# Kernel tuning notes

Hardware: AMD Instinct MI355X
Metric: run time of the kernel (lower is better)

Reference implementation:

```python
import jax, jax.numpy as jnp
import numpy as np

B, L, D, V, K = 4, 2048, 1024, 32, 4096  # batch, seq, embedding_dim, vq_dim, num_embeddings


def setup_inputs() -> dict:
    key = jax.random.key(0)
    k0, k1, k2, k3 = jax.random.split(key, 4)
    h = jax.random.normal(k0, (B, L, D), jnp.float32)
    attn_mask = jnp.ones((B, L), jnp.float32)
    # proj: Linear(D -> V); proj_inv: Linear(V -> D)
    Wp = jax.random.normal(k1, (V, D), jnp.float32) / np.float32(np.sqrt(D))
    bp = jnp.zeros((V,), jnp.float32)
    Wpi = jax.random.normal(k2, (D, V), jnp.float32) / np.float32(np.sqrt(V))
    bpi = jnp.zeros((D,), jnp.float32)
    # embedding init uniform(-1/K, 1/K)
    emb = jax.random.uniform(k3, (K, V), jnp.float32, -1.0 / K, 1.0 / K)
    return {"h": h, "attn_mask": attn_mask, "Wp": Wp, "bp": bp,
            "Wpi": Wpi, "bpi": bpi, "emb": emb}


def reference(h, attn_mask, Wp, bp, Wpi, bpi, emb, temperature=1.0):
    # project + L2 normalize
    hp = jnp.einsum('bld,vd->blv', h, Wp) + bp            # [B,L,V]
    hp = hp / jnp.linalg.norm(hp, axis=-1, keepdims=True)
    # normalize codebook (in torch this is an in-place .data update)
    emb_n = emb / jnp.linalg.norm(emb, axis=-1, keepdims=True)  # [K,V]
    # squared euclidean distances hp vs codebook
    d = (jnp.sum(hp * hp, axis=-1, keepdims=True)
         + jnp.sum(emb_n * emb_n, axis=-1)
         - 2.0 * jnp.einsum('blv,kv->blk', hp, emb_n))    # [B,L,K]
    A = jax.nn.softmax(-d / temperature, axis=-1)         # [B,L,K]
    code = jnp.argmax(A, axis=-1)                         # [B,L]
    h_vq = jnp.einsum('blk,kv->blv', A, emb_n)            # train mode: A @ embedding
    # masked scatter into zeros is equivalent to masking out unselected positions
    m = (attn_mask == 1)
    quantized = jnp.where(m[..., None], h_vq, jnp.float32(0.0))
    vq_code = jnp.where(m, code, 0).astype(jnp.int32)
    quantized = jnp.einsum('blv,dv->bld', quantized, Wpi) + bpi
    vq_loss = jnp.float32(0.0)
    return quantized, vq_code, vq_loss
```

## Files before the change

### kernel.cpp

```cpp
#include <hip/hip_runtime.h>
#include <hip/hip_bf16.h>
#include <math.h>

#define NTOK 8192
#define DIM  1024
#define VDIM 32
#define KCODES 4096

#define SC 2.8853900817779268f

typedef __attribute__((ext_vector_type(8))) short short8;
typedef __attribute__((ext_vector_type(4))) float f32x4;
typedef __attribute__((ext_vector_type(2))) float f32x2;

#define MFMA16(A,B,C) __builtin_amdgcn_mfma_f32_16x16x32_bf16(A, B, C, 0, 0, 0)

__device__ __forceinline__ unsigned short f2bf(float x) {
    unsigned u = __builtin_bit_cast(unsigned, x);
    u += 0x7FFF + ((u >> 16) & 1);
    return (unsigned short)(u >> 16);
}
__device__ __forceinline__ float bf2f(unsigned short b) {
    unsigned u = ((unsigned)b) << 16;
    return __builtin_bit_cast(float, u);
}
__device__ __forceinline__ float fexp2(float x) {
#if __has_builtin(__builtin_amdgcn_exp2f)
    return __builtin_amdgcn_exp2f(x);
#else
    return __expf(0.6931471805599453f * x);
#endif
}

struct U4 { unsigned x, y, z, w; };

__device__ __forceinline__ void split8(const float* p, short8* H, short8* L) {
    unsigned hh[4], ll[4];
    #pragma unroll
    for (int i = 0; i < 4; ++i) {
        unsigned short a = f2bf(p[2 * i]);
        unsigned short b = f2bf(p[2 * i + 1]);
        hh[i] = (unsigned)a | ((unsigned)b << 16);
        unsigned short la = f2bf(p[2 * i] - bf2f(a));
        unsigned short lb = f2bf(p[2 * i + 1] - bf2f(b));
        ll[i] = (unsigned)la | ((unsigned)lb << 16);
    }
    U4 uh = {hh[0], hh[1], hh[2], hh[3]};
    U4 ul = {ll[0], ll[1], ll[2], ll[3]};
    *H = __builtin_bit_cast(short8, uh);
    *L = __builtin_bit_cast(short8, ul);
}

__device__ __forceinline__ short8 pack8(const float* p) {
    unsigned u[8];
    #pragma unroll
    for (int j = 0; j < 8; ++j) u[j] = __builtin_bit_cast(unsigned, p[j]) + 0x8000u;
    U4 uh;
    uh.x = __builtin_amdgcn_perm(u[1], u[0], 0x07060302);
    uh.y = __builtin_amdgcn_perm(u[3], u[2], 0x07060302);
    uh.z = __builtin_amdgcn_perm(u[5], u[4], 0x07060302);
    uh.w = __builtin_amdgcn_perm(u[7], u[6], 0x07060302);
    return __builtin_bit_cast(short8, uh);
}

__device__ __forceinline__ int lsw(int row, int j) {
    int s = ((row >> 1) ^ (row >> 3)) & 3;
    return row * 40 + ((j ^ s) * 8);
}

#define OFS_E_HI   0
#define OFS_E_LO   131072
#define OFS_ET_HI  262144
#define OFS_WP_HI  393216
#define OFS_WP_LO  425984
#define OFS_WPI_HI 458752
#define OFS_WPI_LO 491520
#define OFS_HP_HI  524288
#define OFS_HP_LO  786432
#define F32_BASE   1048576
#define NSPLIT 8
#define FOFS_HVP 0
#define FOFS_LP  2097152
#define FOFS_AMP 2162688
#define FOFS_AIP 2228224

__global__ __launch_bounds__(256) void k_prep(const float* __restrict__ emb,
                                              const float* __restrict__ Wp,
                                              const float* __restrict__ Wpi,
                                              unsigned short* __restrict__ W,
                                              float* __restrict__ loss_out) {
    __shared__ __align__(16) unsigned short Th[32][72];
    int bid = blockIdx.x, tid = threadIdx.x;
    if (bid < 64) {
        int cb = bid * 64;
        int c = tid >> 2, s = tid & 3;
        const float* src = emb + (size_t)(cb + c) * VDIM + s * 8;
        float4 a = *(const float4*)src;
        float4 b = *(const float4*)(src + 4);
        float ps = a.x*a.x + a.y*a.y + a.z*a.z + a.w*a.w
                 + b.x*b.x + b.y*b.y + b.z*b.z + b.w*b.w;
        ps += __shfl_xor(ps, 1);
        ps += __shfl_xor(ps, 2);
        float inv = 1.0f / sqrtf(ps);
        float vals[8] = {a.x*inv, a.y*inv, a.z*inv, a.w*inv,
                         b.x*inv, b.y*inv, b.z*inv, b.w*inv};
        short8 H, L;
        split8(vals, &H, &L);
        *(short8*)(W + OFS_E_HI + (size_t)(cb + c) * VDIM + s * 8) = H;
        *(short8*)(W + OFS_E_LO + (size_t)(cb + c) * VDIM + s * 8) = L;
        #pragma unroll
        for (int j = 0; j < 8; ++j) Th[s * 8 + j][c] = f2bf(vals[j]);
        __syncthreads();
        int row = tid >> 3, seg = tid & 7;
        *(short8*)(W + OFS_ET_HI + (size_t)row * KCODES + cb + seg * 8) =
            *(const short8*)&Th[row][seg * 8];
        if (bid == 0 && tid == 0) loss_out[0] = 0.0f;
    } else if (bid < 80) {
        int i0 = (bid - 64) * 2048 + tid * 8;
        float4 a = *(const float4*)(Wp + i0);
        float4 b = *(const float4*)(Wp + i0 + 4);
        float vals[8] = {a.x, a.y, a.z, a.w, b.x, b.y, b.z, b.w};
        short8 H, L;
        split8(vals, &H, &L);
        *(short8*)(W + OFS_WP_HI + i0) = H;
        *(short8*)(W + OFS_WP_LO + i0) = L;
    } else {
        int i0 = (bid - 80) * 2048 + tid * 8;
        float4 a = *(const float4*)(Wpi + i0);
        float4 b = *(const float4*)(Wpi + i0 + 4);
        float vals[8] = {a.x, a.y, a.z, a.w, b.x, b.y, b.z, b.w};
        short8 H, L;
        split8(vals, &H, &L);
        *(short8*)(W + OFS_WPI_HI + i0) = H;
        *(short8*)(W + OFS_WPI_LO + i0) = L;
    }
}

__global__ __launch_bounds__(256) void k_proj(const float* __restrict__ h,
                                              const unsigned short* __restrict__ W,
                                              const float* __restrict__ bp,
                                              unsigned short* __restrict__ hp_hi,
                                              unsigned short* __restrict__ hp_lo) {
    __shared__ __align__(16) float red[4][16][36];
    const unsigned short* Wp_hi = W + OFS_WP_HI;
    const unsigned short* Wp_lo = W + OFS_WP_LO;
    int tid = threadIdx.x;
    int w = tid >> 6, l = tid & 63, q = l >> 4, m = l & 15;
    int tok0 = blockIdx.x * 16;
    const f32x4 zero4 = {0.f, 0.f, 0.f, 0.f};
    f32x4 acc0 = zero4, acc1 = zero4;
    const float* hb = h + (size_t)(tok0 + m) * DIM + w * 256 + q * 8;
    const unsigned short* w0h = Wp_hi + (size_t)m * DIM + w * 256 + q * 8;
    const unsigned short* w0l = Wp_lo + (size_t)m * DIM + w * 256 + q * 8;
    const unsigned short* w1h = w0h + (size_t)16 * DIM;
    const unsigned short* w1l = w0l + (size_t)16 * DIM;
    #pragma unroll
    for (int c = 0; c < 8; ++c) {
        float4 a = *(const float4*)(hb + c * 32);
        float4 b = *(const float4*)(hb + c * 32 + 4);
        float va[8] = {a.x, a.y, a.z, a.w, b.x, b.y, b.z, b.w};
        short8 Bh, Bl;
        split8(va, &Bh, &Bl);
        short8 A0h = *(const short8*)(w0h + c * 32);
        short8 A0l = *(const short8*)(w0l + c * 32);
        short8 A1h = *(const short8*)(w1h + c * 32);
        short8 A1l = *(const short8*)(w1l + c * 32);
        acc0 = MFMA16(A0l, Bl, acc0); acc0 = MFMA16(A0l, Bh, acc0);
        acc0 = MFMA16(A0h, Bl, acc0); acc0 = MFMA16(A0h, Bh, acc0);
        acc1 = MFMA16(A1l, Bl, acc1); acc1 = MFMA16(A1l, Bh, acc1);
        acc1 = MFMA16(A1h, Bl, acc1); acc1 = MFMA16(A1h, Bh, acc1);
    }
    *(f32x4*)&red[w][m][4 * q]      = acc0;
    *(f32x4*)&red[w][m][16 + 4 * q] = acc1;
    __syncthreads();
    #pragma unroll
    for (int half = 0; half < 2; ++half) {
        int t = (tid >> 5) + half * 8, v = tid & 31;
        float s = bp[v];
        #pragma unroll
        for (int j = 0; j < 4; ++j) s += red[j][t][v];
        float sq = s * s;
        #pragma unroll
        for (int off = 1; off < 32; off <<= 1) sq += __shfl_xor(sq, off);
        float nv = s * (SC / sqrtf(sq));
        unsigned short hb2 = f2bf(nv);
        size_t idx = (size_t)(tok0 + t) * VDIM + v;
        hp_hi[idx] = hb2;
        hp_lo[idx] = f2bf(nv - bf2f(hb2));
    }
}

__global__ __launch_bounds__(256, 2) void k_vq(const unsigned short* __restrict__ W,
                                               float* __restrict__ hvp,
                                               float* __restrict__ lp,
                                               float* __restrict__ amp,
                                               int* __restrict__ aip) {
    __shared__ __align__(16) unsigned short Eh[2][64 * 40];
    __shared__ __align__(16) unsigned short El[2][64 * 40];

    const unsigned short* E_hi  = W + OFS_E_HI;
    const unsigned short* E_lo  = W + OFS_E_LO;
    const unsigned short* Et_hi = W + OFS_ET_HI;
    const unsigned short* hp_hi = W + OFS_HP_HI;
    const unsigned short* hp_lo = W + OFS_HP_LO;

    int tid = threadIdx.x;
    int w = tid >> 6, l = tid & 63, q = l >> 4, m = l & 15;
    int tg = blockIdx.x >> 3, sp = blockIdx.x & 7;
    int tok0 = tg * 128 + w * 32;
    int cb0 = sp * 512;
    int sig = ((m & 12) << 1) | (m & 3);
    const f32x4 zero4 = {0.f, 0.f, 0.f, 0.f};

    int cs = tid >> 2, js = tid & 3;
    int lds_off = lsw(cs, js);
    size_t gs = (size_t)cs * VDIM + js * 8;

    size_t h0 = (size_t)(tok0 + m) * VDIM + q * 8;
    short8 hph0 = *(const short8*)(hp_hi + h0);
    short8 hpl0 = *(const short8*)(hp_lo + h0);
    short8 hph1 = *(const short8*)(hp_hi + h0 + 16 * VDIM);
    short8 hpl1 = *(const short8*)(hp_lo + h0 + 16 * VDIM);

    {
        size_t tb = (size_t)cb0 * VDIM;
        short8 a = *(const short8*)(E_hi + tb + gs);
        short8 b = *(const short8*)(E_lo + tb + gs);
        *(short8*)&Eh[0][lds_off] = a;
        *(short8*)&El[0][lds_off] = b;
    }
    __syncthreads();

    f32x4 hv00 = zero4, hv01 = zero4, hv10 = zero4, hv11 = zero4;
    f32x2 ls0v = {0.f, 0.f}, ls1v = {0.f, 0.f};
    float am0 = -1e30f, am1 = -1e30f;
    int ai0 = 0, ai1 = 0;

    #pragma unroll 1
    for (int t = 0; t < 8; ++t) {
        int buf = t & 1;
        short8 sa, sb;
        if (t < 7) {
            size_t tb = (size_t)(cb0 + (t + 1) * 64) * VDIM;
            sa = *(const short8*)(E_hi + tb + gs);
            sb = *(const short8*)(E_lo + tb + gs);
        }
        int cbase = cb0 + t * 64;
        size_t tb0 = (size_t)sig * KCODES + cbase + q * 8;
        short8 T00 = *(const short8*)(Et_hi + tb0);
        short8 T01 = *(const short8*)(Et_hi + tb0 + (size_t)4 * KCODES);
        short8 T10 = *(const short8*)(Et_hi + tb0 + 32);
        short8 T11 = *(const short8*)(Et_hi + tb0 + 32 + (size_t)4 * KCODES);
        short8 E00h = *(const short8*)&Eh[buf][lsw(sig,          q)];
        short8 E00l = *(const short8*)&El[buf][lsw(sig,          q)];
        short8 E01h = *(const short8*)&Eh[buf][lsw(sig + 4,      q)];
        short8 E01l = *(const short8*)&El[buf][lsw(sig + 4,      q)];
        short8 E10h = *(const short8*)&Eh[buf][lsw(32 + sig,     q)];
        short8 E10l = *(const short8*)&El[buf][lsw(32 + sig,     q)];
        short8 E11h = *(const short8*)&Eh[buf][lsw(32 + sig + 4, q)];
        short8 E11l = *(const short8*)&El[buf][lsw(32 + sig + 4, q)];

        f32x4 sA0, sA1, sB0, sB1, sC0, sC1, sD0, sD1;
        sA0 = MFMA16(E00h, hpl0, zero4);
        sA1 = MFMA16(E01h, hpl0, zero4);
        sB0 = MFMA16(E00h, hpl1, zero4);
        sB1 = MFMA16(E01h, hpl1, zero4);
        sC0 = MFMA16(E10h, hpl0, zero4);
        sC1 = MFMA16(E11h, hpl0, zero4);
        sD0 = MFMA16(E10h, hpl1, zero4);
        sD1 = MFMA16(E11h, hpl1, zero4);
        sA0 = MFMA16(E00l, hph0, sA0);
        sA1 = MFMA16(E01l, hph0, sA1);
        sB0 = MFMA16(E00l, hph1, sB0);
        sB1 = MFMA16(E01l, hph1, sB1);
        sC0 = MFMA16(E10l, hph0, sC0);
        sC1 = MFMA16(E11l, hph0, sC1);
        sD0 = MFMA16(E10l, hph1, sD0);
        sD1 = MFMA16(E11l, hph1, sD1);
        sA0 = MFMA16(E00h, hph0, sA0);
        sA1 = MFMA16(E01h, hph0, sA1);
        sB0 = MFMA16(E00h, hph1, sB0);
        sB1 = MFMA16(E01h, hph1, sB1);
        sC0 = MFMA16(E10h, hph0, sC0);
        sC1 = MFMA16(E11h, hph0, sC1);
        sD0 = MFMA16(E10h, hph1, sD0);
        sD1 = MFMA16(E11h, hph1, sD1);

        {
            int lbase = cbase + 8 * q;
            float p[8];
            #pragma unroll
            for (int r = 0; r < 4; ++r) { p[r] = fexp2(sA0[r]); p[4 + r] = fexp2(sA1[r]); }
            short8 Ph = pack8(p);
            hv00 = MFMA16(T00, Ph, hv00);
            hv01 = MFMA16(T01, Ph, hv01);
            #pragma unroll
            for (int r = 0; r < 4; ++r) {
                float sv = sA0[r];
                if (sv > am0) { am0 = sv; ai0 = lbase + r; }
                sv = sA1[r];
                if (sv > am0) { am0 = sv; ai0 = lbase + 4 + r; }
            }
            f32x2 pa = {p[0], p[1]}, pb = {p[2], p[3]};
            f32x2 pc = {p[4], p[5]}, pd = {p[6], p[7]};
            ls0v += (pa + pb) + (pc + pd);
        }
        {
            int lbase = cbase + 8 * q;
            float p[8];
            #pragma unroll
            for (int r = 0; r < 4; ++r) { p[r] = fexp2(sB0[r]); p[4 + r] = fexp2(sB1[r]); }
            short8 Ph = pack8(p);
            hv10 = MFMA16(T00, Ph, hv10);
            hv11 = MFMA16(T01, Ph, hv11);
            #pragma unroll
            for (int r = 0; r < 4; ++r) {
                float sv = sB0[r];
                if (sv > am1) { am1 = sv; ai1 = lbase + r; }
                sv = sB1[r];
                if (sv > am1) { am1 = sv; ai1 = lbase + 4 + r; }
            }
            f32x2 pa = {p[0], p[1]}, pb = {p[2], p[3]};
            f32x2 pc = {p[4], p[5]}, pd = {p[6], p[7]};
            ls1v += (pa + pb) + (pc + pd);
        }
        {
            int lbase = cbase + 32 + 8 * q;
            float p[8];
            #pragma unroll
            for (int r = 0; r < 4; ++r) { p[r] = fexp2(sC0[r]); p[4 + r] = fexp2(sC1[r]); }
            short8 Ph = pack8(p);
            hv00 = MFMA16(T10, Ph, hv00);
            hv01 = MFMA16(T11, Ph, hv01);
            #pragma unroll
            for (int r = 0; r < 4; ++r) {
                float sv = sC0[r];
                if (sv > am0) { am0 = sv; ai0 = lbase + r; }
                sv = sC1[r];
                if (sv > am0) { am0 = sv; ai0 = lbase + 4 + r; }
            }
            f32x2 pa = {p[0], p[1]}, pb = {p[2], p[3]};
            f32x2 pc = {p[4], p[5]}, pd = {p[6], p[7]};
            ls0v += (pa + pb) + (pc + pd);
        }
        {
            int lbase = cbase + 32 + 8 * q;
            float p[8];
            #pragma unroll
            for (int r = 0; r < 4; ++r) { p[r] = fexp2(sD0[r]); p[4 + r] = fexp2(sD1[r]); }
            short8 Ph = pack8(p);
            hv10 = MFMA16(T10, Ph, hv10);
            hv11 = MFMA16(T11, Ph, hv11);
            #pragma unroll
            for (int r = 0; r < 4; ++r) {
                float sv = sD0[r];
                if (sv > am1) { am1 = sv; ai1 = lbase + r; }
                sv = sD1[r];
                if (sv > am1) { am1 = sv; ai1 = lbase + 4 + r; }
            }
            f32x2 pa = {p[0], p[1]}, pb = {p[2], p[3]};
            f32x2 pc = {p[4], p[5]}, pd = {p[6], p[7]};
            ls1v += (pa + pb) + (pc + pd);
        }

        if (t < 7) {
            int nb = buf ^ 1;
            *(short8*)&Eh[nb][lds_off] = sa;
            *(short8*)&El[nb][lds_off] = sb;
            __syncthreads();
        }
    }

    float ls0 = ls0v.x + ls0v.y;
    float ls1 = ls1v.x + ls1v.y;
    #pragma unroll
    for (int off = 16; off <= 32; off <<= 1) {
        ls0 += __shfl_xor(ls0, off);
        float a2 = __shfl_xor(am0, off);
        int   i2 = __shfl_xor(ai0, off);
        if (a2 > am0 || (a2 == am0 && i2 < ai0)) { am0 = a2; ai0 = i2; }
        ls1 += __shfl_xor(ls1, off);
        a2 = __shfl_xor(am1, off);
        i2 = __shfl_xor(ai1, off);
        if (a2 > am1 || (a2 == am1 && i2 < ai1)) { am1 = a2; ai1 = i2; }
    }
    size_t gtok = (size_t)sp * NTOK + tok0;
    if (q == 0) {
        lp[gtok + m] = ls0;      amp[gtok + m] = am0;      aip[gtok + m] = ai0;
        lp[gtok + 16 + m] = ls1; amp[gtok + 16 + m] = am1; aip[gtok + 16 + m] = ai1;
    }
    float* dst0 = hvp + (gtok + m) * VDIM;
    *(f32x4*)(dst0 + 8 * q)     = hv00;
    *(f32x4*)(dst0 + 8 * q + 4) = hv01;
    float* dst1 = hvp + (gtok + 16 + m) * VDIM;
    *(f32x4*)(dst1 + 8 * q)     = hv10;
    *(f32x4*)(dst1 + 8 * q + 4) = hv11;
}

__global__ __launch_bounds__(256) void k_out(const unsigned short* __restrict__ W,
                                             const float* __restrict__ mask,
                                             const float* __restrict__ bpi,
                                             const float* __restrict__ hvp,
                                             const float* __restrict__ lp,
                                             const float* __restrict__ amp,
                                             const int* __restrict__ aip,
                                             float* __restrict__ out,
                                             float* __restrict__ code_out) {
    __shared__ float invl[16];
    __shared__ float lred[16][9];
    __shared__ float amred[16][9];
    __shared__ int   aired[16][9];
    __shared__ __align__(16) unsigned short hvh[16][40];
    __shared__ __align__(16) unsigned short hvl[16][40];
    const unsigned short* Wpi_hi = W + OFS_WPI_HI;
    const unsigned short* Wpi_lo = W + OFS_WPI_LO;
    int tid = threadIdx.x;
    int tok0 = blockIdx.x * 16;
    const f32x4 zero4 = {0.f, 0.f, 0.f, 0.f};

    if (tid < 128) {
        int t = tid >> 3, s = tid & 7;
        size_t gi = (size_t)s * NTOK + tok0 + t;
        lred[t][s]  = lp[gi];
        amred[t][s] = amp[gi];
        aired[t][s] = aip[gi];
    }
    __syncthreads();
    if (tid < 16) {
        float L = 0.f, A = -1e30f;
        int I = 0x7fffffff;
        #pragma unroll
        for (int s = 0; s < NSPLIT; ++s) {
            L += lred[tid][s];
            float a2 = amred[tid][s];
            int   i2 = aired[tid][s];
            if (a2 > A || (a2 == A && i2 < I)) { A = a2; I = i2; }
        }
        bool on = (mask[tok0 + tid] == 1.0f);
        code_out[tok0 + tid] = on ? (float)I : 0.0f;
        invl[tid] = on ? (1.0f / L) : 0.0f;
    }
    __syncthreads();
    if (tid < 128) {
        int t = tid >> 3, g = tid & 7;
        f32x4 x = zero4;
        #pragma unroll
        for (int sp = 0; sp < NSPLIT; ++sp)
            x += *(const f32x4*)&hvp[((size_t)sp * NTOK + tok0 + t) * VDIM + g * 4];
        float iv = invl[t];
        #pragma unroll
        for (int j = 0; j < 4; ++j) {
            float xv = x[j] * iv;
            unsigned short hb = f2bf(xv);
            hvh[t][g * 4 + j] = hb;
            hvl[t][g * 4 + j] = f2bf(xv - bf2f(hb));
        }
    }
    __syncthreads();
    int w = tid >> 6, l = tid & 63, q = l >> 4, m = l & 15;
    short8 gh = *(const short8*)&hvh[m][q * 8];
    short8 gl = *(const short8*)&hvl[m][q * 8];
    #pragma unroll
    for (int dt = 0; dt < 16; ++dt) {
        int dbase = w * 256 + dt * 16;
        short8 Ah = *(const short8*)(Wpi_hi + (size_t)(dbase + m) * VDIM + q * 8);
        short8 Al = *(const short8*)(Wpi_lo + (size_t)(dbase + m) * VDIM + q * 8);
        f32x4 o = MFMA16(Al, gh, zero4);
        o = MFMA16(Ah, gl, o);
        o = MFMA16(Ah, gh, o);
        float4 bias = *(const float4*)(bpi + dbase + 4 * q);
        float4 r0 = make_float4(o[0] + bias.x, o[1] + bias.y,
                                o[2] + bias.z, o[3] + bias.w);
        *(float4*)(out + (size_t)(tok0 + m) * DIM + dbase + 4 * q) = r0;
    }
}

extern "C" void kernel_launch(void* const* d_in, const int* in_sizes, int n_in,
                              void* d_out, int out_size, void* d_ws, size_t ws_size,
                              hipStream_t stream) {
    const float* h    = (const float*)d_in[0];
    const float* mask = (const float*)d_in[1];
    const float* Wp   = (const float*)d_in[2];
    const float* bp   = (const float*)d_in[3];
    const float* Wpi  = (const float*)d_in[4];
    const float* bpi  = (const float*)d_in[5];
    const float* emb  = (const float*)d_in[6];
    float* out = (float*)d_out;

    unsigned short* W = (unsigned short*)d_ws;
    unsigned short* hp_hi = W + OFS_HP_HI;
    unsigned short* hp_lo = W + OFS_HP_LO;
    float* fbase = (float*)(W + F32_BASE);
    float* hvp = fbase + FOFS_HVP;
    float* lpp = fbase + FOFS_LP;
    float* ampp = fbase + FOFS_AMP;
    int*   aipp = (int*)(fbase + FOFS_AIP);

    float* code_out = out + (size_t)NTOK * DIM;
    float* loss_out = code_out + NTOK;

    hipLaunchKernelGGL(k_prep, dim3(96),  dim3(256), 0, stream, emb, Wp, Wpi, W, loss_out);
    hipLaunchKernelGGL(k_proj, dim3(512), dim3(256), 0, stream, h, W, bp, hp_hi, hp_lo);
    hipLaunchKernelGGL(k_vq,   dim3(512), dim3(256), 0, stream, W, hvp, lpp, ampp, aipp);
    hipLaunchKernelGGL(k_out,  dim3(512), dim3(256), 0, stream, W, mask, bpi, hvp, lpp, ampp, aipp, out, code_out);
}
```

Before: 134.1 us.

## Shrink prep kernel, fold codebook prep into proj, halve vq block size

```diff
diff --git a/kernel.cpp b/kernel.cpp
--- a/kernel.cpp
+++ b/kernel.cpp
@@ -84,67 +84,71 @@
 #define FOFS_AMP 2162688
 #define FOFS_AIP 2228224
 
-__global__ __launch_bounds__(256) void k_prep(const float* __restrict__ emb,
-                                              const float* __restrict__ Wp,
+__global__ __launch_bounds__(256) void k_prep(const float* __restrict__ Wp,
+                                              unsigned short* __restrict__ W,
+                                              float* __restrict__ loss_out) {
+    int bid = blockIdx.x, tid = threadIdx.x;
+    int i0 = bid * 2048 + tid * 8;
+    float4 a = *(const float4*)(Wp + i0);
+    float4 b = *(const float4*)(Wp + i0 + 4);
+    float vals[8] = {a.x, a.y, a.z, a.w, b.x, b.y, b.z, b.w};
+    short8 H, L;
+    split8(vals, &H, &L);
+    *(short8*)(W + OFS_WP_HI + i0) = H;
+    *(short8*)(W + OFS_WP_LO + i0) = L;
+    if (bid == 0 && tid == 0) loss_out[0] = 0.0f;
+}
+
+__global__ __launch_bounds__(256) void k_proj(const float* __restrict__ h,
+                                              const unsigned short* __restrict__ Wr,
+                                              const float* __restrict__ bp,
+                                              const float* __restrict__ emb,
                                               const float* __restrict__ Wpi,
                                               unsigned short* __restrict__ W,
-                                              float* __restrict__ loss_out) {
-    __shared__ __align__(16) unsigned short Th[32][72];
-    int bid = blockIdx.x, tid = threadIdx.x;
-    if (bid < 64) {
-        int cb = bid * 64;
-        int c = tid >> 2, s = tid & 3;
-        const float* src = emb + (size_t)(cb + c) * VDIM + s * 8;
-        float4 a = *(const float4*)src;
-        float4 b = *(const float4*)(src + 4);
-        float ps = a.x*a.x + a.y*a.y + a.z*a.z + a.w*a.w
-                 + b.x*b.x + b.y*b.y + b.z*b.z + b.w*b.w;
-        ps += __shfl_xor(ps, 1);
-        ps += __shfl_xor(ps, 2);
-        float inv = 1.0f / sqrtf(ps);
-        float vals[8] = {a.x*inv, a.y*inv, a.z*inv, a.w*inv,
-                         b.x*inv, b.y*inv, b.z*inv, b.w*inv};
-        short8 H, L;
-        split8(vals, &H, &L);
-        *(short8*)(W + OFS_E_HI + (size_t)(cb + c) * VDIM + s * 8) = H;
-        *(short8*)(W + OFS_E_LO + (size_t)(cb + c) * VDIM + s * 8) = L;
-        #pragma unroll
-        for (int j = 0; j < 8; ++j) Th[s * 8 + j][c] = f2bf(vals[j]);
-        __syncthreads();
-        int row = tid >> 3, seg = tid & 7;
-        *(short8*)(W + OFS_ET_HI + (size_t)row * KCODES + cb + seg * 8) =
-            *(const short8*)&Th[row][seg * 8];
-        if (bid == 0 && tid == 0) loss_out[0] = 0.0f;
-    } else if (bid < 80) {
-        int i0 = (bid - 64) * 2048 + tid * 8;
-        float4 a = *(const float4*)(Wp + i0);
-        float4 b = *(const float4*)(Wp + i0 + 4);
-        float vals[8] = {a.x, a.y, a.z, a.w, b.x, b.y, b.z, b.w};
-        short8 H, L;
-        split8(vals, &H, &L);
-        *(short8*)(W + OFS_WP_HI + i0) = H;
-        *(short8*)(W + OFS_WP_LO + i0) = L;
-    } else {
-        int i0 = (bid - 80) * 2048 + tid * 8;
-        float4 a = *(const float4*)(Wpi + i0);
-        float4 b = *(const float4*)(Wpi + i0 + 4);
-        float vals[8] = {a.x, a.y, a.z, a.w, b.x, b.y, b.z, b.w};
-        short8 H, L;
-        split8(vals, &H, &L);
-        *(short8*)(W + OFS_WPI_HI + i0) = H;
-        *(short8*)(W + OFS_WPI_LO + i0) = L;
-    }
-}
-
-__global__ __launch_bounds__(256) void k_proj(const float* __restrict__ h,
-                                              const unsigned short* __restrict__ W,
-                                              const float* __restrict__ bp,
                                               unsigned short* __restrict__ hp_hi,
                                               unsigned short* __restrict__ hp_lo) {
     __shared__ __align__(16) float red[4][16][36];
-    const unsigned short* Wp_hi = W + OFS_WP_HI;
-    const unsigned short* Wp_lo = W + OFS_WP_LO;
+    __shared__ __align__(16) unsigned short Th[32][72];
     int tid = threadIdx.x;
+    if (blockIdx.x >= 512) {
+        int bid2 = blockIdx.x - 512;
+        if (bid2 < 64) {
+            int cb = bid2 * 64;
+            int c = tid >> 2, s = tid & 3;
+            const float* src = emb + (size_t)(cb + c) * VDIM + s * 8;
+            float4 a = *(const float4*)src;
+            float4 b = *(const float4*)(src + 4);
+            float ps = a.x*a.x + a.y*a.y + a.z*a.z + a.w*a.w
+                     + b.x*b.x + b.y*b.y + b.z*b.z + b.w*b.w;
+            ps += __shfl_xor(ps, 1);
+            ps += __shfl_xor(ps, 2);
+            float inv = 1.0f / sqrtf(ps);
+            float vals[8] = {a.x*inv, a.y*inv, a.z*inv, a.w*inv,
+                             b.x*inv, b.y*inv, b.z*inv, b.w*inv};
+            short8 H, L;
+            split8(vals, &H, &L);
+            *(short8*)(W + OFS_E_HI + (size_t)(cb + c) * VDIM + s * 8) = H;
+            *(short8*)(W + OFS_E_LO + (size_t)(cb + c) * VDIM + s * 8) = L;
+            #pragma unroll
+            for (int j = 0; j < 8; ++j) Th[s * 8 + j][c] = f2bf(vals[j]);
+            __syncthreads();
+            int row = tid >> 3, seg = tid & 7;
+            *(short8*)(W + OFS_ET_HI + (size_t)row * KCODES + cb + seg * 8) =
+                *(const short8*)&Th[row][seg * 8];
+        } else {
+            int i0 = (bid2 - 64) * 2048 + tid * 8;
+            float4 a = *(const float4*)(Wpi + i0);
+            float4 b = *(const float4*)(Wpi + i0 + 4);
+            float vals[8] = {a.x, a.y, a.z, a.w, b.x, b.y, b.z, b.w};
+            short8 H, L;
+            split8(vals, &H, &L);
+            *(short8*)(W + OFS_WPI_HI + i0) = H;
+            *(short8*)(W + OFS_WPI_LO + i0) = L;
+        }
+        return;
+    }
+    const unsigned short* Wp_hi = Wr + OFS_WP_HI;
+    const unsigned short* Wp_lo = Wr + OFS_WP_LO;
     int w = tid >> 6, l = tid & 63, q = l >> 4, m = l & 15;
     int tok0 = blockIdx.x * 16;
     const f32x4 zero4 = {0.f, 0.f, 0.f, 0.f};
@@ -190,7 +194,7 @@
     }
 }
 
-__global__ __launch_bounds__(256, 2) void k_vq(const unsigned short* __restrict__ W,
+__global__ __launch_bounds__(128, 2) void k_vq(const unsigned short* __restrict__ W,
                                                float* __restrict__ hvp,
                                                float* __restrict__ lp,
                                                float* __restrict__ amp,
@@ -207,14 +211,15 @@
     int tid = threadIdx.x;
     int w = tid >> 6, l = tid & 63, q = l >> 4, m = l & 15;
     int tg = blockIdx.x >> 3, sp = blockIdx.x & 7;
-    int tok0 = tg * 128 + w * 32;
+    int tok0 = tg * 64 + w * 32;
     int cb0 = sp * 512;
     int sig = ((m & 12) << 1) | (m & 3);
     const f32x4 zero4 = {0.f, 0.f, 0.f, 0.f};
 
-    int cs = tid >> 2, js = tid & 3;
-    int lds_off = lsw(cs, js);
-    size_t gs = (size_t)cs * VDIM + js * 8;
+    int cs = tid >> 1, jb = (tid & 1) * 2;
+    int lds_o0 = lsw(cs, jb), lds_o1 = lsw(cs, jb + 1);
+    size_t gs0 = (size_t)cs * VDIM + jb * 8;
+    size_t gs1 = gs0 + 8;
 
     size_t h0 = (size_t)(tok0 + m) * VDIM + q * 8;
     short8 hph0 = *(const short8*)(hp_hi + h0);
@@ -224,10 +229,14 @@
 
     {
         size_t tb = (size_t)cb0 * VDIM;
-        short8 a = *(const short8*)(E_hi + tb + gs);
-        short8 b = *(const short8*)(E_lo + tb + gs);
-        *(short8*)&Eh[0][lds_off] = a;
-        *(short8*)&El[0][lds_off] = b;
+        short8 a0 = *(const short8*)(E_hi + tb + gs0);
+        short8 a1 = *(const short8*)(E_hi + tb + gs1);
+        short8 b0 = *(const short8*)(E_lo + tb + gs0);
+        short8 b1 = *(const short8*)(E_lo + tb + gs1);
+        *(short8*)&Eh[0][lds_o0] = a0;
+        *(short8*)&Eh[0][lds_o1] = a1;
+        *(short8*)&El[0][lds_o0] = b0;
+        *(short8*)&El[0][lds_o1] = b1;
     }
     __syncthreads();
 
@@ -239,11 +248,13 @@
     #pragma unroll 1
     for (int t = 0; t < 8; ++t) {
         int buf = t & 1;
-        short8 sa, sb;
+        short8 sa0, sa1, sb0, sb1;
         if (t < 7) {
             size_t tb = (size_t)(cb0 + (t + 1) * 64) * VDIM;
-            sa = *(const short8*)(E_hi + tb + gs);
-            sb = *(const short8*)(E_lo + tb + gs);
+            sa0 = *(const short8*)(E_hi + tb + gs0);
+            sa1 = *(const short8*)(E_hi + tb + gs1);
+            sb0 = *(const short8*)(E_lo + tb + gs0);
+            sb1 = *(const short8*)(E_lo + tb + gs1);
         }
         int cbase = cb0 + t * 64;
         size_t tb0 = (size_t)sig * KCODES + cbase + q * 8;
@@ -365,8 +376,10 @@
 
         if (t < 7) {
             int nb = buf ^ 1;
-            *(short8*)&Eh[nb][lds_off] = sa;
-            *(short8*)&El[nb][lds_off] = sb;
+            *(short8*)&Eh[nb][lds_o0] = sa0;
+            *(short8*)&Eh[nb][lds_o1] = sa1;
+            *(short8*)&El[nb][lds_o0] = sb0;
+            *(short8*)&El[nb][lds_o1] = sb1;
             __syncthreads();
         }
     }
@@ -499,8 +512,8 @@
     float* code_out = out + (size_t)NTOK * DIM;
     float* loss_out = code_out + NTOK;
 
-    hipLaunchKernelGGL(k_prep, dim3(96),  dim3(256), 0, stream, emb, Wp, Wpi, W, loss_out);
-    hipLaunchKernelGGL(k_proj, dim3(512), dim3(256), 0, stream, h, W, bp, hp_hi, hp_lo);
-    hipLaunchKernelGGL(k_vq,   dim3(512), dim3(256), 0, stream, W, hvp, lpp, ampp, aipp);
-    hipLaunchKernelGGL(k_out,  dim3(512), dim3(256), 0, stream, W, mask, bpi, hvp, lpp, ampp, aipp, out, code_out);
-}
+    hipLaunchKernelGGL(k_prep, dim3(16),   dim3(256), 0, stream, Wp, W, loss_out);
+    hipLaunchKernelGGL(k_proj, dim3(592),  dim3(256), 0, stream, h, W, bp, emb, Wpi, W, hp_hi, hp_lo);
+    hipLaunchKernelGGL(k_vq,   dim3(1024), dim3(128), 0, stream, W, hvp, lpp, ampp, aipp);
+    hipLaunchKernelGGL(k_out,  dim3(512),  dim3(256), 0, stream, W, mask, bpi, hvp, lpp, ampp, aipp, out, code_out);
+}
```

Measured after the change: 134.7 us. Within noise of the previous version (+0.5%).

## Fold prep kernel into projection and double tokens per output block

Applied to the files above, without the earlier changes.

```diff
diff --git a/kernel.cpp b/kernel.cpp
--- a/kernel.cpp
+++ b/kernel.cpp
@@ -71,8 +71,6 @@
 #define OFS_E_HI   0
 #define OFS_E_LO   131072
 #define OFS_ET_HI  262144
-#define OFS_WP_HI  393216
-#define OFS_WP_LO  425984
 #define OFS_WPI_HI 458752
 #define OFS_WPI_LO 491520
 #define OFS_HP_HI  524288
@@ -84,76 +82,63 @@
 #define FOFS_AMP 2162688
 #define FOFS_AIP 2228224
 
-__global__ __launch_bounds__(256) void k_prep(const float* __restrict__ emb,
+__global__ __launch_bounds__(256) void k_proj(const float* __restrict__ h,
                                               const float* __restrict__ Wp,
+                                              const float* __restrict__ bp,
+                                              const float* __restrict__ emb,
                                               const float* __restrict__ Wpi,
                                               unsigned short* __restrict__ W,
+                                              unsigned short* __restrict__ hp_hi,
+                                              unsigned short* __restrict__ hp_lo,
                                               float* __restrict__ loss_out) {
+    __shared__ __align__(16) float red[4][16][36];
     __shared__ __align__(16) unsigned short Th[32][72];
-    int bid = blockIdx.x, tid = threadIdx.x;
-    if (bid < 64) {
-        int cb = bid * 64;
-        int c = tid >> 2, s = tid & 3;
-        const float* src = emb + (size_t)(cb + c) * VDIM + s * 8;
-        float4 a = *(const float4*)src;
-        float4 b = *(const float4*)(src + 4);
-        float ps = a.x*a.x + a.y*a.y + a.z*a.z + a.w*a.w
-                 + b.x*b.x + b.y*b.y + b.z*b.z + b.w*b.w;
-        ps += __shfl_xor(ps, 1);
-        ps += __shfl_xor(ps, 2);
-        float inv = 1.0f / sqrtf(ps);
-        float vals[8] = {a.x*inv, a.y*inv, a.z*inv, a.w*inv,
-                         b.x*inv, b.y*inv, b.z*inv, b.w*inv};
-        short8 H, L;
-        split8(vals, &H, &L);
-        *(short8*)(W + OFS_E_HI + (size_t)(cb + c) * VDIM + s * 8) = H;
-        *(short8*)(W + OFS_E_LO + (size_t)(cb + c) * VDIM + s * 8) = L;
-        #pragma unroll
-        for (int j = 0; j < 8; ++j) Th[s * 8 + j][c] = f2bf(vals[j]);
-        __syncthreads();
-        int row = tid >> 3, seg = tid & 7;
-        *(short8*)(W + OFS_ET_HI + (size_t)row * KCODES + cb + seg * 8) =
-            *(const short8*)&Th[row][seg * 8];
-        if (bid == 0 && tid == 0) loss_out[0] = 0.0f;
-    } else if (bid < 80) {
-        int i0 = (bid - 64) * 2048 + tid * 8;
-        float4 a = *(const float4*)(Wp + i0);
-        float4 b = *(const float4*)(Wp + i0 + 4);
-        float vals[8] = {a.x, a.y, a.z, a.w, b.x, b.y, b.z, b.w};
-        short8 H, L;
-        split8(vals, &H, &L);
-        *(short8*)(W + OFS_WP_HI + i0) = H;
-        *(short8*)(W + OFS_WP_LO + i0) = L;
-    } else {
-        int i0 = (bid - 80) * 2048 + tid * 8;
-        float4 a = *(const float4*)(Wpi + i0);
-        float4 b = *(const float4*)(Wpi + i0 + 4);
-        float vals[8] = {a.x, a.y, a.z, a.w, b.x, b.y, b.z, b.w};
-        short8 H, L;
-        split8(vals, &H, &L);
-        *(short8*)(W + OFS_WPI_HI + i0) = H;
-        *(short8*)(W + OFS_WPI_LO + i0) = L;
-    }
-}
-
-__global__ __launch_bounds__(256) void k_proj(const float* __restrict__ h,
-                                              const unsigned short* __restrict__ W,
-                                              const float* __restrict__ bp,
-                                              unsigned short* __restrict__ hp_hi,
-                                              unsigned short* __restrict__ hp_lo) {
-    __shared__ __align__(16) float red[4][16][36];
-    const unsigned short* Wp_hi = W + OFS_WP_HI;
-    const unsigned short* Wp_lo = W + OFS_WP_LO;
     int tid = threadIdx.x;
+    if (blockIdx.x >= 512) {
+        int bid2 = blockIdx.x - 512;
+        if (bid2 < 64) {
+            int cb = bid2 * 64;
+            int c = tid >> 2, s = tid & 3;
+            const float* src = emb + (size_t)(cb + c) * VDIM + s * 8;
+            float4 a = *(const float4*)src;
+            float4 b = *(const float4*)(src + 4);
+            float ps = a.x*a.x + a.y*a.y + a.z*a.z + a.w*a.w
+                     + b.x*b.x + b.y*b.y + b.z*b.z + b.w*b.w;
+            ps += __shfl_xor(ps, 1);
+            ps += __shfl_xor(ps, 2);
+            float inv = 1.0f / sqrtf(ps);
+            float vals[8] = {a.x*inv, a.y*inv, a.z*inv, a.w*inv,
+                             b.x*inv, b.y*inv, b.z*inv, b.w*inv};
+            short8 H, L;
+            split8(vals, &H, &L);
+            *(short8*)(W + OFS_E_HI + (size_t)(cb + c) * VDIM + s * 8) = H;
+            *(short8*)(W + OFS_E_LO + (size_t)(cb + c) * VDIM + s * 8) = L;
+            #pragma unroll
+            for (int j = 0; j < 8; ++j) Th[s * 8 + j][c] = f2bf(vals[j]);
+            __syncthreads();
+            int row = tid >> 3, seg = tid & 7;
+            *(short8*)(W + OFS_ET_HI + (size_t)row * KCODES + cb + seg * 8) =
+                *(const short8*)&Th[row][seg * 8];
+            if (bid2 == 0 && tid == 0) loss_out[0] = 0.0f;
+        } else {
+            int i0 = (bid2 - 64) * 2048 + tid * 8;
+            float4 a = *(const float4*)(Wpi + i0);
+            float4 b = *(const float4*)(Wpi + i0 + 4);
+            float vals[8] = {a.x, a.y, a.z, a.w, b.x, b.y, b.z, b.w};
+            short8 H, L;
+            split8(vals, &H, &L);
+            *(short8*)(W + OFS_WPI_HI + i0) = H;
+            *(short8*)(W + OFS_WPI_LO + i0) = L;
+        }
+        return;
+    }
     int w = tid >> 6, l = tid & 63, q = l >> 4, m = l & 15;
     int tok0 = blockIdx.x * 16;
     const f32x4 zero4 = {0.f, 0.f, 0.f, 0.f};
     f32x4 acc0 = zero4, acc1 = zero4;
     const float* hb = h + (size_t)(tok0 + m) * DIM + w * 256 + q * 8;
-    const unsigned short* w0h = Wp_hi + (size_t)m * DIM + w * 256 + q * 8;
-    const unsigned short* w0l = Wp_lo + (size_t)m * DIM + w * 256 + q * 8;
-    const unsigned short* w1h = w0h + (size_t)16 * DIM;
-    const unsigned short* w1l = w0l + (size_t)16 * DIM;
+    const float* wp0 = Wp + (size_t)m * DIM + w * 256 + q * 8;
+    const float* wp1 = wp0 + (size_t)16 * DIM;
     #pragma unroll
     for (int c = 0; c < 8; ++c) {
         float4 a = *(const float4*)(hb + c * 32);
@@ -161,10 +146,16 @@
         float va[8] = {a.x, a.y, a.z, a.w, b.x, b.y, b.z, b.w};
         short8 Bh, Bl;
         split8(va, &Bh, &Bl);
-        short8 A0h = *(const short8*)(w0h + c * 32);
-        short8 A0l = *(const short8*)(w0l + c * 32);
-        short8 A1h = *(const short8*)(w1h + c * 32);
-        short8 A1l = *(const short8*)(w1l + c * 32);
+        float4 w0a = *(const float4*)(wp0 + c * 32);
+        float4 w0b = *(const float4*)(wp0 + c * 32 + 4);
+        float v0[8] = {w0a.x, w0a.y, w0a.z, w0a.w, w0b.x, w0b.y, w0b.z, w0b.w};
+        short8 A0h, A0l;
+        split8(v0, &A0h, &A0l);
+        float4 w1a = *(const float4*)(wp1 + c * 32);
+        float4 w1b = *(const float4*)(wp1 + c * 32 + 4);
+        float v1[8] = {w1a.x, w1a.y, w1a.z, w1a.w, w1b.x, w1b.y, w1b.z, w1b.w};
+        short8 A1h, A1l;
+        split8(v1, &A1h, &A1l);
         acc0 = MFMA16(A0l, Bl, acc0); acc0 = MFMA16(A0l, Bh, acc0);
         acc0 = MFMA16(A0h, Bl, acc0); acc0 = MFMA16(A0h, Bh, acc0);
         acc1 = MFMA16(A1l, Bl, acc1); acc1 = MFMA16(A1l, Bh, acc1);
@@ -406,19 +397,19 @@
                                              const int* __restrict__ aip,
                                              float* __restrict__ out,
                                              float* __restrict__ code_out) {
-    __shared__ float invl[16];
-    __shared__ float lred[16][9];
-    __shared__ float amred[16][9];
-    __shared__ int   aired[16][9];
-    __shared__ __align__(16) unsigned short hvh[16][40];
-    __shared__ __align__(16) unsigned short hvl[16][40];
+    __shared__ float invl[32];
+    __shared__ float lred[32][9];
+    __shared__ float amred[32][9];
+    __shared__ int   aired[32][9];
+    __shared__ __align__(16) unsigned short hvh[32][40];
+    __shared__ __align__(16) unsigned short hvl[32][40];
     const unsigned short* Wpi_hi = W + OFS_WPI_HI;
     const unsigned short* Wpi_lo = W + OFS_WPI_LO;
     int tid = threadIdx.x;
-    int tok0 = blockIdx.x * 16;
+    int tok0 = blockIdx.x * 32;
     const f32x4 zero4 = {0.f, 0.f, 0.f, 0.f};
 
-    if (tid < 128) {
+    {
         int t = tid >> 3, s = tid & 7;
         size_t gi = (size_t)s * NTOK + tok0 + t;
         lred[t][s]  = lp[gi];
@@ -426,7 +417,7 @@
         aired[t][s] = aip[gi];
     }
     __syncthreads();
-    if (tid < 16) {
+    if (tid < 32) {
         float L = 0.f, A = -1e30f;
         int I = 0x7fffffff;
         #pragma unroll
@@ -441,7 +432,7 @@
         invl[tid] = on ? (1.0f / L) : 0.0f;
     }
     __syncthreads();
-    if (tid < 128) {
+    {
         int t = tid >> 3, g = tid & 7;
         f32x4 x = zero4;
         #pragma unroll
@@ -458,20 +449,28 @@
     }
     __syncthreads();
     int w = tid >> 6, l = tid & 63, q = l >> 4, m = l & 15;
-    short8 gh = *(const short8*)&hvh[m][q * 8];
-    short8 gl = *(const short8*)&hvl[m][q * 8];
+    short8 gh0 = *(const short8*)&hvh[m][q * 8];
+    short8 gl0 = *(const short8*)&hvl[m][q * 8];
+    short8 gh1 = *(const short8*)&hvh[16 + m][q * 8];
+    short8 gl1 = *(const short8*)&hvl[16 + m][q * 8];
     #pragma unroll
     for (int dt = 0; dt < 16; ++dt) {
         int dbase = w * 256 + dt * 16;
         short8 Ah = *(const short8*)(Wpi_hi + (size_t)(dbase + m) * VDIM + q * 8);
         short8 Al = *(const short8*)(Wpi_lo + (size_t)(dbase + m) * VDIM + q * 8);
-        f32x4 o = MFMA16(Al, gh, zero4);
-        o = MFMA16(Ah, gl, o);
-        o = MFMA16(Ah, gh, o);
         float4 bias = *(const float4*)(bpi + dbase + 4 * q);
-        float4 r0 = make_float4(o[0] + bias.x, o[1] + bias.y,
-                                o[2] + bias.z, o[3] + bias.w);
+        f32x4 o0 = MFMA16(Al, gh0, zero4);
+        o0 = MFMA16(Ah, gl0, o0);
+        o0 = MFMA16(Ah, gh0, o0);
+        f32x4 o1 = MFMA16(Al, gh1, zero4);
+        o1 = MFMA16(Ah, gl1, o1);
+        o1 = MFMA16(Ah, gh1, o1);
+        float4 r0 = make_float4(o0[0] + bias.x, o0[1] + bias.y,
+                                o0[2] + bias.z, o0[3] + bias.w);
         *(float4*)(out + (size_t)(tok0 + m) * DIM + dbase + 4 * q) = r0;
+        float4 r1 = make_float4(o1[0] + bias.x, o1[1] + bias.y,
+                                o1[2] + bias.z, o1[3] + bias.w);
+        *(float4*)(out + (size_t)(tok0 + 16 + m) * DIM + dbase + 4 * q) = r1;
     }
 }
 
@@ -499,8 +498,7 @@
     float* code_out = out + (size_t)NTOK * DIM;
     float* loss_out = code_out + NTOK;
 
-    hipLaunchKernelGGL(k_prep, dim3(96),  dim3(256), 0, stream, emb, Wp, Wpi, W, loss_out);
-    hipLaunchKernelGGL(k_proj, dim3(512), dim3(256), 0, stream, h, W, bp, hp_hi, hp_lo);
+    hipLaunchKernelGGL(k_proj, dim3(592), dim3(256), 0, stream, h, Wp, bp, emb, Wpi, W, hp_hi, hp_lo, loss_out);
     hipLaunchKernelGGL(k_vq,   dim3(512), dim3(256), 0, stream, W, hvp, lpp, ampp, aipp);
-    hipLaunchKernelGGL(k_out,  dim3(512), dim3(256), 0, stream, W, mask, bpi, hvp, lpp, ampp, aipp, out, code_out);
-}
+    hipLaunchKernelGGL(k_out,  dim3(256), dim3(256), 0, stream, W, mask, bpi, hvp, lpp, ampp, aipp, out, code_out);
+}
```

After: 128.3 us. 4.3% less time.
